# Optimization experiments

Measured on AMD Instinct MI355X. Metric: run time of the kernel, lower is better.

The kernel has to match this reference:

```python
import jax, jax.numpy as jnp
import numpy as np

B, P, ENC, DEC, EMB, ATT, FFN, V, MAXLEN = 64, 196, 512, 512, 256, 128, 1024, 2000, 160
T = MAXLEN - 1
EPS = 1e-5

def _k(i):
    return jax.random.fold_in(jax.random.key(0), i)

def _w(i, shape):
    return jax.random.normal(_k(i), shape, jnp.float32) * 0.02

def setup_inputs() -> dict:
    lens = jnp.concatenate([jnp.array([MAXLEN]), jax.random.randint(_k(2), (B - 1,), 2, MAXLEN + 1)])
    return {
        "encoder_out": jax.random.normal(_k(0), (B, P, ENC), jnp.float32),
        "encoded_captions": jax.random.randint(_k(1), (B, MAXLEN), 0, V),
        "caption_lengths": lens,
        "enc_att_w": _w(3, (ATT, ENC)), "enc_att_b": _w(4, (ATT,)),
        "dec_att_w": _w(5, (ATT, DEC)), "dec_att_b": _w(6, (ATT,)),
        "full_att_w": _w(7, (1, ATT)), "full_att_b": _w(8, (1,)),
        "gate_w1": _w(9, (ATT, DEC)), "gate_b1": _w(10, (ATT,)),
        "gate_w2": _w(11, (1, ATT)), "gate_b2": _w(12, (1,)),
        "emb": jax.random.uniform(_k(13), (V, EMB), jnp.float32, -0.1, 0.1),
        "gru1_wih": _w(14, (3 * DEC, EMB + ENC)), "gru1_whh": _w(15, (3 * DEC, DEC)),
        "gru1_bih": _w(16, (3 * DEC,)), "gru1_bhh": _w(17, (3 * DEC,)),
        "gru2_wih": _w(18, (3 * DEC, DEC)), "gru2_whh": _w(19, (3 * DEC, DEC)),
        "gru2_bih": _w(20, (3 * DEC,)), "gru2_bhh": _w(21, (3 * DEC,)),
        "proj_w": _w(22, (DEC, EMB + ENC)), "proj_b": _w(23, (DEC,)),
        "ln1_g": jnp.ones((DEC,), jnp.float32), "ln1_b": jnp.zeros((DEC,), jnp.float32),
        "ln2_g": jnp.ones((DEC,), jnp.float32), "ln2_b": jnp.zeros((DEC,), jnp.float32),
        "ffn_w1": _w(24, (FFN, DEC)), "ffn_b1": jnp.zeros((FFN,), jnp.float32),
        "ffn_w2": _w(25, (V, FFN)), "ffn_b2": jnp.zeros((V,), jnp.float32),
    }

def _gru(x, h, wih, whh, bih, bhh):
    gi = x @ wih.T + bih
    gh = h @ whh.T + bhh
    ir, iz, ig = jnp.split(gi, 3, axis=-1)
    hr, hz, hg = jnp.split(gh, 3, axis=-1)
    r = jax.nn.sigmoid(ir + hr)
    z = jax.nn.sigmoid(iz + hz)
    n = jnp.tanh(ig + r * hg)
    return (1.0 - z) * n + z * h

def _ln(x, g, b):
    m = x.mean(-1, keepdims=True)
    v = x.var(-1, keepdims=True)
    return (x - m) / jnp.sqrt(v + EPS) * g + b

def _decode(encoder_out, encoded_captions, caption_lengths,
            enc_att_w, enc_att_b, dec_att_w, dec_att_b, full_att_w, full_att_b,
            gate_w1, gate_b1, gate_w2, gate_b2, emb,
            gru1_wih, gru1_whh, gru1_bih, gru1_bhh,
            gru2_wih, gru2_whh, gru2_bih, gru2_bhh,
            proj_w, proj_b, ln1_g, ln1_b, ln2_g, ln2_b,
            ffn_w1, ffn_b1, ffn_w2, ffn_b2):
    # sort by caption length descending (packed-sequence style)
    order = jnp.argsort(-caption_lengths)
    enc = encoder_out[order]                       # [B,P,ENC]
    caps = encoded_captions[order]                 # [B,MAXLEN]
    dec_lens = caption_lengths[order] - 1          # [B]
    att1 = enc @ enc_att_w.T + enc_att_b           # [B,P,ATT] (loop-invariant)
    xs = jnp.swapaxes(emb[caps[:, :T]], 0, 1)      # [T,B,EMB] teacher forcing (p=1.0)
    masks = (jnp.arange(T)[:, None] < dec_lens[None, :]).astype(enc.dtype)  # [T,B]

    def step(carry, inp):
        h1, h2 = carry
        x_t, m = inp                               # [B,EMB], [B]
        att2 = h2 @ dec_att_w.T + dec_att_b        # [B,ATT]
        e = (jax.nn.relu(att1 + att2[:, None, :]) @ full_att_w.T + full_att_b)[..., 0]  # [B,P]
        alpha = jax.nn.softmax(e, axis=1)
        awe = jnp.einsum('bpe,bp->be', enc, alpha)
        gate = jax.nn.sigmoid(jax.nn.relu(h2 @ gate_w1.T + gate_b1) @ gate_w2.T + gate_b2)  # [B,1]
        awe = awe * gate
        gin = jnp.concatenate([x_t, awe], axis=1)  # [B,EMB+ENC]
        h1_new = _gru(gin, h1, gru1_wih, gru1_whh, gru1_bih, gru1_bhh)
        h1_res = _ln(h1_new + gin @ proj_w.T + proj_b, ln1_g, ln1_b)
        h2_new = _gru(h1_res, h2, gru2_wih, gru2_whh, gru2_bih, gru2_bhh)
        h2_res = _ln(h2_new + h1_res, ln2_g, ln2_b)  # dropout is identity (eval)
        preds = jax.nn.relu(h2_res @ ffn_w1.T + ffn_b1) @ ffn_w2.T + ffn_b2  # [B,V]
        mc = m[:, None]
        h1 = jnp.where(mc > 0, h1_new, h1)
        h2 = jnp.where(mc > 0, h2_new, h2)
        return (h1, h2), (preds * mc, alpha * mc)

    h0 = jnp.zeros((enc.shape[0], DEC), enc.dtype)
    _, (preds, alphas) = jax.lax.scan(step, (h0, h0), (xs, masks))
    predictions = jnp.swapaxes(preds, 0, 1)        # [B,T,V]
    alphas = jnp.swapaxes(alphas, 0, 1)            # [B,T,P]
    return predictions, caps, dec_lens, alphas, order

def reference(encoder_out, encoded_captions, caption_lengths,
              enc_att_w, enc_att_b, dec_att_w, dec_att_b, full_att_w, full_att_b,
              gate_w1, gate_b1, gate_w2, gate_b2, emb,
              gru1_wih, gru1_whh, gru1_bih, gru1_bhh,
              gru2_wih, gru2_whh, gru2_bih, gru2_bhh,
              proj_w, proj_b, ln1_g, ln1_b, ln2_g, ln2_b,
              ffn_w1, ffn_b1, ffn_w2, ffn_b2):
    return _decode(encoder_out, encoded_captions, caption_lengths,
                   enc_att_w, enc_att_b, dec_att_w, dec_att_b, full_att_w, full_att_b,
                   gate_w1, gate_b1, gate_w2, gate_b2, emb,
                   gru1_wih, gru1_whh, gru1_bih, gru1_bhh,
                   gru2_wih, gru2_whh, gru2_bih, gru2_bhh,
                   proj_w, proj_b, ln1_g, ln1_b, ln2_g, ln2_b,
                   ffn_w1, ffn_b1, ffn_w2, ffn_b2)
```

## Files before the change

### kernel.cpp

```cpp
#include <hip/hip_runtime.h>
#include <math.h>

#define B 64
#define P 196
#define ENCD 512
#define DECD 512
#define EMBD 256
#define ATTD 128
#define FFND 1024
#define VV 2000
#define MAXLEN 160
#define TSTEPS 159
#define EPS 1e-5f

#define OUT_PRED ((size_t)0)
#define OUT_CAPS ((size_t)(B * TSTEPS * VV))
#define OUT_DECL (OUT_CAPS + (size_t)(B * MAXLEN))
#define OUT_ALPH (OUT_DECL + (size_t)B)
#define OUT_ORDR (OUT_ALPH + (size_t)(B * TSTEPS * P))


struct Ctx {
  const float* enc; const int* caps_in; const int* lens_in;
  const float* eaw; const float* eab; const float* daw; const float* dab;
  const float* faw; const float* fab;
  const float* gw1; const float* gb1; const float* gw2; const float* gb2;
  const float* emb;
  const float* wih1; const float* whh1; const float* bih1; const float* bhh1;
  const float* wih2; const float* whh2; const float* bih2; const float* bhh2;
  const float* projw; const float* projb;
  const float* ln1g; const float* ln1b; const float* ln2g; const float* ln2b;
  const float* fw1; const float* fb1; const float* fw2; const float* fb2;
  int* leafs; int* root;
  int* order_i; int* declen; int* caps_s;
  float* EaT; float* att1;
  float* h1; float* h2; float* v1; float* v2;
  float* gin; float* fgr; float* gh1g; float* gh2g; float* att2acc;
  float* stats1; float* stats2;
  unsigned int* WA; unsigned int* WB; unsigned int* WC; unsigned int* WD;
  float* Watt;
  float* Sf; float* cbf; float* Sg; float* cbg;
  float* out;
};

__device__ __forceinline__ float sigf(float x) { return 1.f / (1.f + __expf(-x)); }

__device__ __forceinline__ float ld4(const float* p) {
  unsigned int u = __hip_atomic_load((const unsigned int*)p, __ATOMIC_RELAXED, __HIP_MEMORY_SCOPE_AGENT);
  return __uint_as_float(u);
}
__device__ __forceinline__ void st4(float* p, float v) {
  __hip_atomic_store((unsigned int*)p, __float_as_uint(v), __ATOMIC_RELAXED, __HIP_MEMORY_SCOPE_AGENT);
}
__device__ __forceinline__ void st8(float* p, float a, float b2) {
  unsigned long long v = ((unsigned long long)__float_as_uint(b2) << 32) | (unsigned long long)__float_as_uint(a);
  __hip_atomic_store((unsigned long long*)p, v, __ATOMIC_RELAXED, __HIP_MEMORY_SCOPE_AGENT);
}
__device__ __forceinline__ void atomF(float* p, float v) {
  __hip_atomic_fetch_add(p, v, __ATOMIC_RELAXED, __HIP_MEMORY_SCOPE_AGENT);
}
__device__ __forceinline__ float4 ldg16(const float* p) {
  float4 d;
  asm volatile("global_load_dwordx4 %0, %1, off sc0 sc1" : "=v"(d) : "v"(p));
  return d;
}
__device__ __forceinline__ void vmwait() { asm volatile("s_waitcnt vmcnt(0)" ::: "memory"); }

__device__ __forceinline__ unsigned short tobf(float x) {
  unsigned int u = __float_as_uint(x);
  u += 0x7fffu + ((u >> 16) & 1u);
  return (unsigned short)(u >> 16);
}
__device__ __forceinline__ float frombf(unsigned short s) {
  return __uint_as_float(((unsigned int)s) << 16);
}
__device__ __forceinline__ unsigned int pack2bf(float a, float b) {
  return (unsigned int)tobf(a) | ((unsigned int)tobf(b) << 16);
}
__device__ __forceinline__ void bf2(unsigned int u, float& a, float& b) {
  a = __uint_as_float(u << 16);
  b = __uint_as_float(u & 0xffff0000u);
}


__global__ void k_order(Ctx c) {
  __shared__ int lens[B];
  int tid = threadIdx.x;
  lens[tid] = c.lens_in[tid];
  __syncthreads();
  int li = lens[tid];
  int pos = 0;
  for (int j = 0; j < B; ++j) {
    int lj = lens[j];
    pos += (lj > li || (lj == li && j < tid)) ? 1 : 0;
  }
  c.order_i[pos] = tid;
  c.declen[pos] = li - 1;
  c.out[OUT_ORDR + pos] = (float)tid;
  c.out[OUT_DECL + pos] = (float)(li - 1);
}

__global__ __launch_bounds__(256) void k_caps(Ctx c) {
  int idx = blockIdx.x * 256 + threadIdx.x;
  if (idx < B * MAXLEN) {
    int b = idx / MAXLEN, t = idx - b * MAXLEN;
    int v = c.caps_in[c.order_i[b] * MAXLEN + t];
    c.caps_s[idx] = v;
    c.out[OUT_CAPS + idx] = (float)v;
  }
}

__global__ __launch_bounds__(256) void k_eat(Ctx c) {
  int idx = blockIdx.x * 256 + threadIdx.x;
  if (idx < 128 * 512) {
    int k = idx >> 7, d = idx & 127;
    c.EaT[(size_t)k * 128 + d] = c.eaw[(size_t)d * 512 + k];
  }
}

__global__ __launch_bounds__(256) void k_att1(Ctx c) {
  __shared__ float Xs[8 * 512];
  int tid = threadIdx.x;
  int r0 = blockIdx.x * 8;
  for (int idx = tid; idx < 8 * 512; idx += 256) {
    int rr = idx >> 9, k = idx & 511;
    int r = r0 + rr;
    int b = r / P, p = r - b * P;
    int ob = c.order_i[b];
    Xs[idx] = c.enc[((size_t)(ob * P + p)) * ENCD + k];
  }
  __syncthreads();
  int d = tid >> 1, kh = tid & 1;
  float acc[8];
#pragma unroll
  for (int rr = 0; rr < 8; ++rr) acc[rr] = 0.f;
  int kbase = kh * 256;
  for (int k = 0; k < 256; ++k) {
    float w = c.EaT[(size_t)(kbase + k) * 128 + d];
#pragma unroll
    for (int rr = 0; rr < 8; ++rr) acc[rr] = fmaf(w, Xs[rr * 512 + kbase + k], acc[rr]);
  }
#pragma unroll
  for (int rr = 0; rr < 8; ++rr) {
    acc[rr] += __shfl_xor(acc[rr], 1);
    if (kh == 0) c.att1[(size_t)(r0 + rr) * 128 + d] = acc[rr];
  }
}

__device__ __forceinline__ float wa_elem(const Ctx& c, int col, int k) {
  if (col < 1536) return c.whh1[(size_t)col * 512 + k];
  if (col < 3072) return c.whh2[(size_t)(col - 1536) * 512 + k];
  return c.ln2g[k] * c.fw1[(size_t)(col - 3072) * 512 + k];
}

__global__ __launch_bounds__(256) void k_wpa(Ctx c) {
  int s = blockIdx.x;
  unsigned int* dst = c.WA + (size_t)s * 32768;
  for (int idx = threadIdx.x; idx < 32768; idx += 256) {
    int kb8 = idx >> 9, r = idx & 511, cc = r >> 2, jw = r & 3;
    int col = s * 128 + cc, k0 = kb8 * 8 + jw * 2;
    dst[idx] = pack2bf(wa_elem(c, col, k0), wa_elem(c, col, k0 + 1));
  }
}

__device__ __forceinline__ float wb_elem(const Ctx& c, int u, int k) {
  int d = u >> 2, comp = u & 3;
  return (comp < 3) ? c.wih1[(size_t)(comp * 512 + d) * 768 + k]
                    : c.projw[(size_t)d * 768 + k];
}

__global__ __launch_bounds__(256) void k_wpb(Ctx c) {
  int s = blockIdx.x;
  unsigned int* dst = c.WB + (size_t)s * 24576;
  for (int idx = threadIdx.x; idx < 24576; idx += 256) {
    int kb8 = idx >> 8, r = idx & 255, cc = r >> 2, jw = r & 3;
    int u = s * 64 + cc, k0 = kb8 * 8 + jw * 2;
    dst[idx] = pack2bf(wb_elem(c, u, k0), wb_elem(c, u, k0 + 1));
  }
}

__device__ __forceinline__ float wc_elem(const Ctx& c, int u, int k) {
  int d = u / 3, comp = u - d * 3;
  return c.ln1g[k] * c.wih2[(size_t)(comp * 512 + d) * 512 + k];
}

__global__ __launch_bounds__(256) void k_wpc(Ctx c) {
  int s = blockIdx.x;
  unsigned int* dst = c.WC + (size_t)s * 12288;
  for (int idx = threadIdx.x; idx < 12288; idx += 256) {
    int kb8 = idx / 192, r = idx - kb8 * 192, cc = r >> 2, jw = r & 3;
    int u = s * 48 + cc, k0 = kb8 * 8 + jw * 2;
    dst[idx] = pack2bf(wc_elem(c, u, k0), wc_elem(c, u, k0 + 1));
  }
}

__device__ __forceinline__ float wd_elem(const Ctx& c, int vcol, int k) {
  return (vcol < 2000) ? c.fw2[(size_t)vcol * 1024 + k] : 0.f;
}

__global__ __launch_bounds__(256) void k_wpd(Ctx c) {
  int s = blockIdx.x;
  unsigned int* dst = c.WD + (size_t)s * 32768;
  for (int idx = threadIdx.x; idx < 32768; idx += 256) {
    int kb8 = idx >> 8, r = idx & 255, cc = r >> 2, jw = r & 3;
    int vcol = s * 64 + cc, k0 = kb8 * 8 + jw * 2;
    dst[idx] = pack2bf(wd_elem(c, vcol, k0), wd_elem(c, vcol, k0 + 1));
  }
}

__global__ __launch_bounds__(256) void k_watt(Ctx c) {
  int ks = blockIdx.x;
  float* dst = c.Watt + (size_t)ks * 16384;
  for (int idx = threadIdx.x; idx < 16384; idx += 256) {
    int kb = idx >> 10, r = idx & 1023, cc = r >> 2, jj = r & 3;
    int k = ks * 64 + kb * 4 + jj;
    dst[idx] = (cc < 128) ? c.daw[(size_t)cc * 512 + k] : c.gw1[(size_t)(cc - 128) * 512 + k];
  }
}

__global__ __launch_bounds__(256) void k_consts(Ctx c) {
  __shared__ float r1[256], r2[256];
  int i = blockIdx.x, tid = threadIdx.x;
  float a = 0.f, b2 = 0.f;
  if (i < 1024) {
    const float* w = c.fw1 + (size_t)i * 512;
    for (int k = tid; k < 512; k += 256) {
      a += frombf(tobf(c.ln2g[k] * w[k]));
      b2 = fmaf(c.ln2b[k], w[k], b2);
    }
  } else {
    const float* w = c.wih2 + (size_t)(i - 1024) * 512;
    for (int k = tid; k < 512; k += 256) {
      a += frombf(tobf(c.ln1g[k] * w[k]));
      b2 = fmaf(c.ln1b[k], w[k], b2);
    }
  }
  r1[tid] = a; r2[tid] = b2;
  __syncthreads();
  for (int s = 128; s > 0; s >>= 1) {
    if (tid < s) { r1[tid] += r1[tid + s]; r2[tid] += r2[tid + s]; }
    __syncthreads();
  }
  if (tid == 0) {
    if (i < 1024) { c.Sf[i] = r1[0]; c.cbf[i] = r2[0] + c.fb1[i]; }
    else { c.Sg[i - 1024] = r1[0]; c.cbg[i - 1024] = r2[0] + c.bih2[i - 1024]; }
  }
}


__device__ __forceinline__ void gridbar(int* leafs, int* root, int ph) {
  __builtin_amdgcn_s_waitcnt(0);
  __syncthreads();
  if (threadIdx.x == 0) {
    int old = __hip_atomic_fetch_add(&leafs[(blockIdx.x & 7) * 32], 1,
                                     __ATOMIC_RELAXED, __HIP_MEMORY_SCOPE_AGENT);
    if (old == ph * 32 - 1)
      __hip_atomic_fetch_add(root, 1, __ATOMIC_RELAXED, __HIP_MEMORY_SCOPE_AGENT);
    while (__hip_atomic_load(root, __ATOMIC_RELAXED, __HIP_MEMORY_SCOPE_AGENT) < ph * 8)
      __builtin_amdgcn_s_sleep(1);
  }
  __syncthreads();
}

__global__ __launch_bounds__(512) void persist(Ctx c) {
  __shared__ unsigned short att1L[196 * 130];
  __shared__ unsigned short encL[196 * 128];
  __shared__ float SH[12288];
  __shared__ float eL[256];
  __shared__ float alphaL[256];
  __shared__ float att2sL[128], fawL[128], dabL[128], gb1L[128], gw2L[128];
  __shared__ float wred[16];
  __shared__ float sstat[16];
  __shared__ int declenI[64];
  __shared__ float gb2v, fabv;

  const int g = blockIdx.x;
  const int tid = threadIdx.x;
  const int cg = g & 31;
  const int rg = g >> 5;
  const int r0 = rg * 8;
  const int bA = g >> 2, q = g & 3;
  const int kc = tid >> 6;
  const int ct = tid & 63;

  if (tid < 128) {
    fawL[tid] = c.faw[tid];
    dabL[tid] = c.dab[tid] + c.eab[tid];
    gb1L[tid] = c.gb1[tid];
    gw2L[tid] = c.gw2[tid];
  }
  if (tid == 0) { gb2v = c.gb2[0]; fabv = c.fab[0]; }
  if (tid < 64) declenI[tid] = c.declen[tid];
  {
    const int ob = c.order_i[bA];
    for (int idx = tid; idx < 196 * 128; idx += 512) {
      int p = idx >> 7, j = idx & 127;
      att1L[p * 130 + j] = tobf(c.att1[((size_t)bA * P + p) * 128 + j]);
      encL[idx] = tobf(c.enc[((size_t)(ob * P + p)) * 512 + q * 128 + j]);
    }
  }
  __syncthreads();

  int ph = 0;
  for (int t = 0; t < MAXLEN; ++t) {
    {
      float* XS = SH;
      float* RED = SH + 4096;
      const float* hsrc = ((cg < 12) ? c.h1 : (cg < 24) ? c.h2 : c.v2) + (size_t)r0 * 512;
      float4 s0 = ldg16(hsrc + tid * 4);
      float4 s1 = ldg16(hsrc + 2048 + tid * 4);
      if (tid < 8) {
        int slot = (t + 1) & 1;
        float a = ld4(c.stats2 + slot * 128 + (r0 + tid) * 2);
        float b2 = ld4(c.stats2 + slot * 128 + (r0 + tid) * 2 + 1);
        float m = a * (1.f / 512.f);
        float va = b2 * (1.f / 512.f) - m * m;
        sstat[tid] = m; sstat[8 + tid] = rsqrtf(va + EPS);
      }
      vmwait();
      *(float4*)(XS + tid * 4) = s0;
      *(float4*)(XS + 2048 + tid * 4) = s1;
      __syncthreads();

      {
        const unsigned int* wp = c.WA + (size_t)cg * 32768 + (size_t)kc * 4096 + ct * 4;
        const float* xb = XS + kc * 64;
        float acc[8][2];
#pragma unroll
        for (int r = 0; r < 8; ++r) { acc[r][0] = 0.f; acc[r][1] = 0.f; }
#pragma unroll 2
        for (int i = 0; i < 8; ++i) {
          uint4 u0 = *(const uint4*)(wp + i * 512);
          uint4 u1 = *(const uint4*)(wp + i * 512 + 256);
          float wa[8], wb[8];
          bf2(u0.x, wa[0], wa[1]); bf2(u0.y, wa[2], wa[3]);
          bf2(u0.z, wa[4], wa[5]); bf2(u0.w, wa[6], wa[7]);
          bf2(u1.x, wb[0], wb[1]); bf2(u1.y, wb[2], wb[3]);
          bf2(u1.z, wb[4], wb[5]); bf2(u1.w, wb[6], wb[7]);
#pragma unroll
          for (int r = 0; r < 8; ++r) {
            float4 x0 = *(const float4*)(xb + r * 512 + i * 8);
            float4 x1 = *(const float4*)(xb + r * 512 + i * 8 + 4);
            acc[r][0] = fmaf(wa[0], x0.x, fmaf(wa[1], x0.y, fmaf(wa[2], x0.z, fmaf(wa[3], x0.w, acc[r][0]))));
            acc[r][0] = fmaf(wa[4], x1.x, fmaf(wa[5], x1.y, fmaf(wa[6], x1.z, fmaf(wa[7], x1.w, acc[r][0]))));
            acc[r][1] = fmaf(wb[0], x0.x, fmaf(wb[1], x0.y, fmaf(wb[2], x0.z, fmaf(wb[3], x0.w, acc[r][1]))));
            acc[r][1] = fmaf(wb[4], x1.x, fmaf(wb[5], x1.y, fmaf(wb[6], x1.z, fmaf(wb[7], x1.w, acc[r][1]))));
          }
        }
#pragma unroll
        for (int r = 0; r < 8; ++r) {
          RED[(kc * 8 + r) * 128 + ct] = acc[r][0];
          RED[(kc * 8 + r) * 128 + ct + 64] = acc[r][1];
        }
      }
      if (cg >= 16 && cg < 24) {
        const int ks_att = cg - 16;
        const int ct2 = tid >> 1, half = tid & 1;
        const float* wp = c.Watt + (size_t)ks_att * 16384 + half * 8192 + ct2 * 4;
        const float* xb = XS + ks_att * 64 + half * 32;
        float a[8];
#pragma unroll
        for (int r = 0; r < 8; ++r) a[r] = 0.f;
#pragma unroll
        for (int i = 0; i < 8; ++i) {
          float4 w = *(const float4*)(wp + i * 1024);
#pragma unroll
          for (int r = 0; r < 8; ++r) {
            float4 x = *(const float4*)(xb + r * 512 + i * 4);
            a[r] = fmaf(w.x, x.x, fmaf(w.y, x.y, fmaf(w.z, x.z, fmaf(w.w, x.w, a[r]))));
          }
        }
#pragma unroll
        for (int r = 0; r < 8; ++r) {
          a[r] += __shfl_xor(a[r], 1);
          if (half == 0) atomF(c.att2acc + (r0 + r) * 256 + ct2, a[r]);
        }
      }
      __syncthreads();
      {
        int row = tid >> 6, cp = (tid & 63) * 2;
        float s0_ = 0.f, s1_ = 0.f;
#pragma unroll
        for (int k8 = 0; k8 < 8; ++k8) {
          float2 v = *(const float2*)(RED + (k8 * 8 + row) * 128 + cp);
          s0_ += v.x; s1_ += v.y;
        }
        int bb = r0 + row;
        int gcol = cg * 128 + cp;
        if (cg < 12) st8(c.gh1g + bb * 1536 + gcol, s0_, s1_);
        else if (cg < 24) st8(c.gh2g + bb * 1536 + (gcol - 1536), s0_, s1_);
        else {
          int cf = gcol - 3072;
          float m2 = sstat[row], i2 = sstat[8 + row];
          float v0 = i2 * (s0_ - m2 * c.Sf[cf]) + c.cbf[cf];
          float v1v = i2 * (s1_ - m2 * c.Sf[cf + 1]) + c.cbf[cf + 1];
          st8(c.fgr + bb * 1024 + cf, fmaxf(v0, 0.f), fmaxf(v1v, 0.f));
        }
      }
    }
    gridbar(c.leafs, c.root, ++ph);

    {
      float* XS = SH;
      float* RED = SH + 8192;
      const float* fsrc = c.fgr + (size_t)r0 * 1024;
      float4 s0 = ldg16(fsrc + tid * 4);
      float4 s1 = ldg16(fsrc + 2048 + tid * 4);
      float4 s2 = ldg16(fsrc + 4096 + tid * 4);
      float4 s3 = ldg16(fsrc + 6144 + tid * 4);
      float a2r = 0.f, g1r = 0.f;
      if (tid < 128) {
        a2r = ld4(c.att2acc + bA * 256 + tid);
        g1r = ld4(c.att2acc + bA * 256 + 128 + tid);
      }
      if (g == 0) {
        int sl = t & 1;
        if (tid < 128) st4(c.stats1 + sl * 128 + tid, 0.f);
        else if (tid < 256) st4(c.stats2 + sl * 128 + (tid - 128), 0.f);
      }
      vmwait();
      *(float4*)(XS + tid * 4) = s0;
      *(float4*)(XS + 2048 + tid * 4) = s1;
      *(float4*)(XS + 4096 + tid * 4) = s2;
      *(float4*)(XS + 6144 + tid * 4) = s3;
      if (tid < 128) {
        att2sL[tid] = a2r + dabL[tid];
        float g1 = fmaxf(g1r + gb1L[tid], 0.f);
        float gv = g1 * gw2L[tid];
#pragma unroll
        for (int w = 1; w < 64; w <<= 1) gv += __shfl_xor(gv, w);
        if ((tid & 63) == 0) wred[tid >> 6] = gv;
      }
      __syncthreads();

      {
        const unsigned int* wp = c.WD + (size_t)cg * 32768 + (size_t)kc * 4096 + ct * 4;
        const float* xb = XS + kc * 128;
        float acc[8];
#pragma unroll
        for (int r = 0; r < 8; ++r) acc[r] = 0.f;
#pragma unroll 4
        for (int i = 0; i < 16; ++i) {
          uint4 u = *(const uint4*)(wp + i * 256);
          float w8[8];
          bf2(u.x, w8[0], w8[1]); bf2(u.y, w8[2], w8[3]);
          bf2(u.z, w8[4], w8[5]); bf2(u.w, w8[6], w8[7]);
#pragma unroll
          for (int r = 0; r < 8; ++r) {
            float4 x0 = *(const float4*)(xb + r * 1024 + i * 8);
            float4 x1 = *(const float4*)(xb + r * 1024 + i * 8 + 4);
            acc[r] = fmaf(w8[0], x0.x, fmaf(w8[1], x0.y, fmaf(w8[2], x0.z, fmaf(w8[3], x0.w, acc[r]))));
            acc[r] = fmaf(w8[4], x1.x, fmaf(w8[5], x1.y, fmaf(w8[6], x1.z, fmaf(w8[7], x1.w, acc[r]))));
          }
        }
#pragma unroll
        for (int r = 0; r < 8; ++r) RED[(kc * 8 + r) * 64 + ct] = acc[r];
      }
      __syncthreads();
      {
        int row = tid >> 6, cl = tid & 63;
        float s = 0.f;
#pragma unroll
        for (int k8 = 0; k8 < 8; ++k8) s += RED[(k8 * 8 + row) * 64 + cl];
        int bb = r0 + row, vcol = cg * 64 + cl;
        if (vcol < 2000 && t > 0 && (t - 1) < declenI[bb])
          c.out[OUT_PRED + ((size_t)bb * TSTEPS + (t - 1)) * VV + vcol] = s + c.fb2[vcol];
      }
      {
        int p = tid >> 1, jh = tid & 1;
        float e = 0.f;
        if (p < 196) {
          const unsigned short* ap = att1L + p * 130 + jh * 64;
#pragma unroll 8
          for (int j = 0; j < 64; ++j)
            e = fmaf(fmaxf(frombf(ap[j]) + att2sL[jh * 64 + j], 0.f), fawL[jh * 64 + j], e);
        }
        e += __shfl_xor(e, 1);
        if (jh == 0 && p < 196) eL[p] = e + fabv;
      }
      __syncthreads();
      float ev = (tid < 196) ? eL[tid] : -3.0e38f;
      if (tid < 256) {
        float mv = ev;
#pragma unroll
        for (int w = 1; w < 64; w <<= 1) mv = fmaxf(mv, __shfl_xor(mv, w));
        if ((tid & 63) == 0) wred[2 + (tid >> 6)] = mv;
      }
      __syncthreads();
      float mx = fmaxf(fmaxf(wred[2], wred[3]), fmaxf(wred[4], wred[5]));
      float ex = (tid < 196) ? __expf(ev - mx) : 0.f;
      if (tid < 256) {
        float sv = ex;
#pragma unroll
        for (int w = 1; w < 64; w <<= 1) sv += __shfl_xor(sv, w);
        if ((tid & 63) == 0) wred[6 + (tid >> 6)] = sv;
      }
      __syncthreads();
      float inv = 1.f / (wred[6] + wred[7] + wred[8] + wred[9]);
      float gate = sigf(wred[0] + wred[1] + gb2v);
      if (tid < 256) alphaL[tid] = ex * inv;
      if (q == 0 && tid < 196 && t < declenI[bA])
        c.out[OUT_ALPH + ((size_t)bA * TSTEPS + t) * P + tid] = ex * inv;
      __syncthreads();
      {
        int el = tid & 127, pq = tid >> 7;
        const unsigned short* ep2 = encL + (size_t)(pq * 49) * 128 + el;
        const float* alp = alphaL + pq * 49;
        float s_ = 0.f;
#pragma unroll
        for (int i = 0; i < 49; ++i) s_ = fmaf(alp[i], frombf(ep2[(size_t)i * 128]), s_);
        RED[tid] = s_;
      }
      __syncthreads();
      if (tid < 128) {
        float aw = RED[tid] + RED[128 + tid] + RED[256 + tid] + RED[384 + tid];
        st4(c.gin + bA * 768 + 256 + q * 128 + tid, aw * gate);
      }
      if (q == 1 && tid < 256) {
        int tok = c.caps_s[bA * MAXLEN + t];
        st4(c.gin + bA * 768 + tid, c.emb[(size_t)tok * 256 + tid]);
      }
    }
    gridbar(c.leafs, c.root, ++ph);

    {
      float* XS = SH;
      float* RED = SH + 6144;
      const float* gsrc = c.gin + (size_t)r0 * 768;
      float4 s0 = ldg16(gsrc + tid * 4);
      float4 s1 = ldg16(gsrc + 2048 + tid * 4);
      float4 s2 = ldg16(gsrc + 4096 + tid * 4);
      if (g < 32) st4(c.att2acc + g * 512 + tid, 0.f);
      vmwait();
      *(float4*)(XS + tid * 4) = s0;
      *(float4*)(XS + 2048 + tid * 4) = s1;
      *(float4*)(XS + 4096 + tid * 4) = s2;
      __syncthreads();

      {
        const unsigned int* wp = c.WB + (size_t)cg * 24576 + (size_t)kc * 3072 + ct * 4;
        const float* xb = XS + kc * 96;
        float acc[8];
#pragma unroll
        for (int r = 0; r < 8; ++r) acc[r] = 0.f;
#pragma unroll 4
        for (int i = 0; i < 12; ++i) {
          uint4 u = *(const uint4*)(wp + i * 256);
          float w8[8];
          bf2(u.x, w8[0], w8[1]); bf2(u.y, w8[2], w8[3]);
          bf2(u.z, w8[4], w8[5]); bf2(u.w, w8[6], w8[7]);
#pragma unroll
          for (int r = 0; r < 8; ++r) {
            float4 x0 = *(const float4*)(xb + r * 768 + i * 8);
            float4 x1 = *(const float4*)(xb + r * 768 + i * 8 + 4);
            acc[r] = fmaf(w8[0], x0.x, fmaf(w8[1], x0.y, fmaf(w8[2], x0.z, fmaf(w8[3], x0.w, acc[r]))));
            acc[r] = fmaf(w8[4], x1.x, fmaf(w8[5], x1.y, fmaf(w8[6], x1.z, fmaf(w8[7], x1.w, acc[r]))));
          }
        }
#pragma unroll
        for (int r = 0; r < 8; ++r) RED[(kc * 8 + r) * 64 + ct] = acc[r];
      }
      __syncthreads();
      if (tid < 128) {
        int row = tid >> 4, dl = tid & 15;
        int bb = r0 + row, d = cg * 16 + dl;
        float gi0 = 0.f, gi1 = 0.f, gi2v = 0.f, gi3 = 0.f;
#pragma unroll
        for (int k8 = 0; k8 < 8; ++k8) {
          float4 v = *(const float4*)(RED + (k8 * 8 + row) * 64 + dl * 4);
          gi0 += v.x; gi1 += v.y; gi2v += v.z; gi3 += v.w;
        }
        float gir = gi0 + c.bih1[d];
        float giz = gi1 + c.bih1[512 + d];
        float gig = gi2v + c.bih1[1024 + d];
        float pj = gi3 + c.projb[d];
        float hr = ld4(c.gh1g + bb * 1536 + d) + c.bhh1[d];
        float hz = ld4(c.gh1g + bb * 1536 + 512 + d) + c.bhh1[512 + d];
        float hg = ld4(c.gh1g + bb * 1536 + 1024 + d) + c.bhh1[1024 + d];
        float r_ = sigf(gir + hr);
        float z_ = sigf(giz + hz);
        float n_ = tanhf(gig + r_ * hg);
        float hold = ld4(c.h1 + bb * 512 + d);
        float hnew = (1.f - z_) * n_ + z_ * hold;
        st4(c.h1 + bb * 512 + d, (t < declenI[bb]) ? hnew : hold);
        float v1v = hnew + pj;
        st4(c.v1 + bb * 512 + d, v1v);
        float ss = v1v, sq = v1v * v1v;
#pragma unroll
        for (int w = 1; w < 16; w <<= 1) { ss += __shfl_xor(ss, w); sq += __shfl_xor(sq, w); }
        if (dl == 0) {
          atomF(c.stats1 + (t & 1) * 128 + bb * 2, ss);
          atomF(c.stats1 + (t & 1) * 128 + bb * 2 + 1, sq);
        }
      }
    }
    gridbar(c.leafs, c.root, ++ph);

    {
      float* XS = SH;
      float* RED = SH + 4096;
      const float* vsrc = c.v1 + (size_t)r0 * 512;
      float4 s0 = ldg16(vsrc + tid * 4);
      float4 s1 = ldg16(vsrc + 2048 + tid * 4);
      if (tid < 8) {
        float a = ld4(c.stats1 + (t & 1) * 128 + (r0 + tid) * 2);
        float b2 = ld4(c.stats1 + (t & 1) * 128 + (r0 + tid) * 2 + 1);
        float m = a * (1.f / 512.f);
        float va = b2 * (1.f / 512.f) - m * m;
        sstat[tid] = m; sstat[8 + tid] = rsqrtf(va + EPS);
      }
      vmwait();
      *(float4*)(XS + tid * 4) = s0;
      *(float4*)(XS + 2048 + tid * 4) = s1;
      __syncthreads();

      if (ct < 48) {
        const unsigned int* wp = c.WC + (size_t)cg * 12288 + (size_t)kc * 1536 + ct * 4;
        const float* xb = XS + kc * 64;
        float acc[8];
#pragma unroll
        for (int r = 0; r < 8; ++r) acc[r] = 0.f;
#pragma unroll 2
        for (int i = 0; i < 8; ++i) {
          uint4 u = *(const uint4*)(wp + i * 192);
          float w8[8];
          bf2(u.x, w8[0], w8[1]); bf2(u.y, w8[2], w8[3]);
          bf2(u.z, w8[4], w8[5]); bf2(u.w, w8[6], w8[7]);
#pragma unroll
          for (int r = 0; r < 8; ++r) {
            float4 x0 = *(const float4*)(xb + r * 512 + i * 8);
            float4 x1 = *(const float4*)(xb + r * 512 + i * 8 + 4);
            acc[r] = fmaf(w8[0], x0.x, fmaf(w8[1], x0.y, fmaf(w8[2], x0.z, fmaf(w8[3], x0.w, acc[r]))));
            acc[r] = fmaf(w8[4], x1.x, fmaf(w8[5], x1.y, fmaf(w8[6], x1.z, fmaf(w8[7], x1.w, acc[r]))));
          }
        }
#pragma unroll
        for (int r = 0; r < 8; ++r) RED[(kc * 8 + r) * 48 + ct] = acc[r];
      }
      __syncthreads();
      if (tid < 128) {
        int row = tid >> 4, dl = tid & 15;
        int bb = r0 + row, d = cg * 16 + dl;
        float gi0 = 0.f, gi1 = 0.f, gi2v = 0.f;
#pragma unroll
        for (int k8 = 0; k8 < 8; ++k8) {
          const float* rp = RED + (k8 * 8 + row) * 48 + dl * 3;
          gi0 += rp[0]; gi1 += rp[1]; gi2v += rp[2];
        }
        float m1 = sstat[row], i1 = sstat[8 + row];
        float gir = i1 * (gi0 - m1 * c.Sg[d]) + c.cbg[d];
        float giz = i1 * (gi1 - m1 * c.Sg[512 + d]) + c.cbg[512 + d];
        float gig = i1 * (gi2v - m1 * c.Sg[1024 + d]) + c.cbg[1024 + d];
        float hr = ld4(c.gh2g + bb * 1536 + d) + c.bhh2[d];
        float hz = ld4(c.gh2g + bb * 1536 + 512 + d) + c.bhh2[512 + d];
        float hg = ld4(c.gh2g + bb * 1536 + 1024 + d) + c.bhh2[1024 + d];
        float r_ = sigf(gir + hr);
        float z_ = sigf(giz + hz);
        float n_ = tanhf(gig + r_ * hg);
        float hold = ld4(c.h2 + bb * 512 + d);
        float hnew = (1.f - z_) * n_ + z_ * hold;
        st4(c.h2 + bb * 512 + d, (t < declenI[bb]) ? hnew : hold);
        float h1r = (XS[row * 512 + d] - m1) * i1 * c.ln1g[d] + c.ln1b[d];
        float v2v = hnew + h1r;
        st4(c.v2 + bb * 512 + d, v2v);
        float ss = v2v, sq = v2v * v2v;
#pragma unroll
        for (int w = 1; w < 16; w <<= 1) { ss += __shfl_xor(ss, w); sq += __shfl_xor(sq, w); }
        if (dl == 0) {
          atomF(c.stats2 + (t & 1) * 128 + bb * 2, ss);
          atomF(c.stats2 + (t & 1) * 128 + bb * 2 + 1, sq);
        }
      }
    }
    gridbar(c.leafs, c.root, ++ph);
  }
}

extern "C" void kernel_launch(void* const* d_in, const int* in_sizes, int n_in,
                              void* d_out, int out_size, void* d_ws, size_t ws_size,
                              hipStream_t stream) {
  (void)in_sizes; (void)n_in; (void)ws_size;
  Ctx c;
  c.enc = (const float*)d_in[0];
  c.caps_in = (const int*)d_in[1];
  c.lens_in = (const int*)d_in[2];
  c.eaw = (const float*)d_in[3];
  c.eab = (const float*)d_in[4];
  c.daw = (const float*)d_in[5];
  c.dab = (const float*)d_in[6];
  c.faw = (const float*)d_in[7];
  c.fab = (const float*)d_in[8];
  c.gw1 = (const float*)d_in[9];
  c.gb1 = (const float*)d_in[10];
  c.gw2 = (const float*)d_in[11];
  c.gb2 = (const float*)d_in[12];
  c.emb = (const float*)d_in[13];
  c.wih1 = (const float*)d_in[14];
  c.whh1 = (const float*)d_in[15];
  c.bih1 = (const float*)d_in[16];
  c.bhh1 = (const float*)d_in[17];
  c.wih2 = (const float*)d_in[18];
  c.whh2 = (const float*)d_in[19];
  c.bih2 = (const float*)d_in[20];
  c.bhh2 = (const float*)d_in[21];
  c.projw = (const float*)d_in[22];
  c.projb = (const float*)d_in[23];
  c.ln1g = (const float*)d_in[24];
  c.ln1b = (const float*)d_in[25];
  c.ln2g = (const float*)d_in[26];
  c.ln2b = (const float*)d_in[27];
  c.fw1 = (const float*)d_in[28];
  c.fb1 = (const float*)d_in[29];
  c.fw2 = (const float*)d_in[30];
  c.fb2 = (const float*)d_in[31];
  c.out = (float*)d_out;

  char* wp_ = (char*)d_ws;
  auto alloc = [&](size_t bytes) -> char* {
    char* p = wp_;
    wp_ += (bytes + 255) & ~(size_t)255;
    return p;
  };
  char* zbase = wp_;
  c.leafs = (int*)alloc(256 * 4);
  c.root = (int*)alloc(256);
  c.h1 = (float*)alloc((size_t)B * 512 * 4);
  c.h2 = (float*)alloc((size_t)B * 512 * 4);
  c.stats1 = (float*)alloc(2 * 64 * 2 * 4);
  c.stats2 = (float*)alloc(2 * 64 * 2 * 4);
  c.att2acc = (float*)alloc((size_t)B * 256 * 4);
  c.v2 = (float*)alloc((size_t)B * 512 * 4);
  size_t zbytes = (size_t)(wp_ - zbase);

  c.order_i = (int*)alloc(B * 4);
  c.declen = (int*)alloc(B * 4);
  c.caps_s = (int*)alloc((size_t)B * MAXLEN * 4);
  c.EaT = (float*)alloc((size_t)512 * 128 * 4);
  c.att1 = (float*)alloc((size_t)B * P * 128 * 4);
  c.v1 = (float*)alloc((size_t)B * 512 * 4);
  c.gin = (float*)alloc((size_t)B * 768 * 4);
  c.fgr = (float*)alloc((size_t)B * 1024 * 4);
  c.gh1g = (float*)alloc((size_t)B * 1536 * 4);
  c.gh2g = (float*)alloc((size_t)B * 1536 * 4);
  c.WA = (unsigned int*)alloc((size_t)32 * 32768 * 4);
  c.WB = (unsigned int*)alloc((size_t)32 * 24576 * 4);
  c.WC = (unsigned int*)alloc((size_t)32 * 12288 * 4);
  c.WD = (unsigned int*)alloc((size_t)32 * 32768 * 4);
  c.Watt = (float*)alloc((size_t)8 * 16384 * 4);
  c.Sf = (float*)alloc(1024 * 4);
  c.cbf = (float*)alloc(1024 * 4);
  c.Sg = (float*)alloc(1536 * 4);
  c.cbg = (float*)alloc(1536 * 4);

  hipMemsetAsync(d_out, 0, (size_t)out_size * 4, stream);
  hipMemsetAsync(zbase, 0, zbytes, stream);

  k_order<<<1, 64, 0, stream>>>(c);
  k_caps<<<(B * MAXLEN + 255) / 256, 256, 0, stream>>>(c);
  k_eat<<<(128 * 512 + 255) / 256, 256, 0, stream>>>(c);
  k_att1<<<(B * P) / 8, 256, 0, stream>>>(c);
  k_wpa<<<32, 256, 0, stream>>>(c);
  k_wpb<<<32, 256, 0, stream>>>(c);
  k_wpc<<<32, 256, 0, stream>>>(c);
  k_wpd<<<32, 256, 0, stream>>>(c);
  k_watt<<<8, 256, 0, stream>>>(c);
  k_consts<<<2560, 256, 0, stream>>>(c);

  persist<<<256, 512, 0, stream>>>(c);
}
```

Before: 11.72 ms.

## Double persistent kernel block size, splitting batch rows across thread halves

Grows the persistent kernel from 512 to 1024 threads per block. Each thread now computes 4 of the 8 batch rows in the bf16 matvec phases, so per-thread accumulator count and serial work are halved. Reduction and epilogue steps are restricted to the first 512 threads. Every thread still loads the same weights, so global weight traffic per block doubles, and the 1024-thread launch bound squeezes the register budget, which risks spills and lower wave occupancy.

```diff
diff --git a/kernel.cpp b/kernel.cpp
--- a/kernel.cpp
+++ b/kernel.cpp
@@ -262,7 +262,7 @@
   __syncthreads();
 }
 
-__global__ __launch_bounds__(512) void persist(Ctx c) {
+__global__ __launch_bounds__(1024) void persist(Ctx c) {
   __shared__ unsigned short att1L[196 * 130];
   __shared__ unsigned short encL[196 * 128];
   __shared__ float SH[12288];
@@ -280,7 +280,8 @@
   const int rg = g >> 5;
   const int r0 = rg * 8;
   const int bA = g >> 2, q = g & 3;
-  const int kc = tid >> 6;
+  const int kc = (tid >> 6) & 7;
+  const int rh = tid >> 9;
   const int ct = tid & 63;
 
   if (tid < 128) {
@@ -293,7 +294,7 @@
   if (tid < 64) declenI[tid] = c.declen[tid];
   {
     const int ob = c.order_i[bA];
-    for (int idx = tid; idx < 196 * 128; idx += 512) {
+    for (int idx = tid; idx < 196 * 128; idx += 1024) {
       int p = idx >> 7, j = idx & 127;
       att1L[p * 130 + j] = tobf(c.att1[((size_t)bA * P + p) * 128 + j]);
       encL[idx] = tobf(c.enc[((size_t)(ob * P + p)) * 512 + q * 128 + j]);
@@ -307,8 +308,7 @@
       float* XS = SH;
       float* RED = SH + 4096;
       const float* hsrc = ((cg < 12) ? c.h1 : (cg < 24) ? c.h2 : c.v2) + (size_t)r0 * 512;
-      float4 s0 = ldg16(hsrc + tid * 4);
-      float4 s1 = ldg16(hsrc + 2048 + tid * 4);
+      float4 sA = ldg16(hsrc + tid * 4);
       if (tid < 8) {
         int slot = (t + 1) & 1;
         float a = ld4(c.stats2 + slot * 128 + (r0 + tid) * 2);
@@ -318,16 +318,15 @@
         sstat[tid] = m; sstat[8 + tid] = rsqrtf(va + EPS);
       }
       vmwait();
-      *(float4*)(XS + tid * 4) = s0;
-      *(float4*)(XS + 2048 + tid * 4) = s1;
+      *(float4*)(XS + tid * 4) = sA;
       __syncthreads();
 
       {
         const unsigned int* wp = c.WA + (size_t)cg * 32768 + (size_t)kc * 4096 + ct * 4;
-        const float* xb = XS + kc * 64;
-        float acc[8][2];
-#pragma unroll
-        for (int r = 0; r < 8; ++r) { acc[r][0] = 0.f; acc[r][1] = 0.f; }
+        const float* xb = XS + (rh * 4) * 512 + kc * 64;
+        float acc[4][2];
+#pragma unroll
+        for (int r = 0; r < 4; ++r) { acc[r][0] = 0.f; acc[r][1] = 0.f; }
 #pragma unroll 2
         for (int i = 0; i < 8; ++i) {
           uint4 u0 = *(const uint4*)(wp + i * 512);
@@ -338,7 +337,7 @@
           bf2(u1.x, wb[0], wb[1]); bf2(u1.y, wb[2], wb[3]);
           bf2(u1.z, wb[4], wb[5]); bf2(u1.w, wb[6], wb[7]);
 #pragma unroll
-          for (int r = 0; r < 8; ++r) {
+          for (int r = 0; r < 4; ++r) {
             float4 x0 = *(const float4*)(xb + r * 512 + i * 8);
             float4 x1 = *(const float4*)(xb + r * 512 + i * 8 + 4);
             acc[r][0] = fmaf(wa[0], x0.x, fmaf(wa[1], x0.y, fmaf(wa[2], x0.z, fmaf(wa[3], x0.w, acc[r][0]))));
@@ -348,12 +347,12 @@
           }
         }
 #pragma unroll
-        for (int r = 0; r < 8; ++r) {
-          RED[(kc * 8 + r) * 128 + ct] = acc[r][0];
-          RED[(kc * 8 + r) * 128 + ct + 64] = acc[r][1];
-        }
-      }
-      if (cg >= 16 && cg < 24) {
+        for (int r = 0; r < 4; ++r) {
+          RED[(kc * 8 + rh * 4 + r) * 128 + ct] = acc[r][0];
+          RED[(kc * 8 + rh * 4 + r) * 128 + ct + 64] = acc[r][1];
+        }
+      }
+      if (cg >= 16 && cg < 24 && tid < 512) {
         const int ks_att = cg - 16;
         const int ct2 = tid >> 1, half = tid & 1;
         const float* wp = c.Watt + (size_t)ks_att * 16384 + half * 8192 + ct2 * 4;
@@ -377,7 +376,7 @@
         }
       }
       __syncthreads();
-      {
+      if (tid < 512) {
         int row = tid >> 6, cp = (tid & 63) * 2;
         float s0_ = 0.f, s1_ = 0.f;
 #pragma unroll
@@ -405,9 +404,7 @@
       float* RED = SH + 8192;
       const float* fsrc = c.fgr + (size_t)r0 * 1024;
       float4 s0 = ldg16(fsrc + tid * 4);
-      float4 s1 = ldg16(fsrc + 2048 + tid * 4);
-      float4 s2 = ldg16(fsrc + 4096 + tid * 4);
-      float4 s3 = ldg16(fsrc + 6144 + tid * 4);
+      float4 s1 = ldg16(fsrc + 4096 + tid * 4);
       float a2r = 0.f, g1r = 0.f;
       if (tid < 128) {
         a2r = ld4(c.att2acc + bA * 256 + tid);
@@ -420,9 +417,7 @@
       }
       vmwait();
       *(float4*)(XS + tid * 4) = s0;
-      *(float4*)(XS + 2048 + tid * 4) = s1;
-      *(float4*)(XS + 4096 + tid * 4) = s2;
-      *(float4*)(XS + 6144 + tid * 4) = s3;
+      *(float4*)(XS + 4096 + tid * 4) = s1;
       if (tid < 128) {
         att2sL[tid] = a2r + dabL[tid];
         float g1 = fmaxf(g1r + gb1L[tid], 0.f);
@@ -435,10 +430,10 @@
 
       {
         const unsigned int* wp = c.WD + (size_t)cg * 32768 + (size_t)kc * 4096 + ct * 4;
-        const float* xb = XS + kc * 128;
-        float acc[8];
-#pragma unroll
-        for (int r = 0; r < 8; ++r) acc[r] = 0.f;
+        const float* xb = XS + (rh * 4) * 1024 + kc * 128;
+        float acc[4];
+#pragma unroll
+        for (int r = 0; r < 4; ++r) acc[r] = 0.f;
 #pragma unroll 4
         for (int i = 0; i < 16; ++i) {
           uint4 u = *(const uint4*)(wp + i * 256);
@@ -446,7 +441,7 @@
           bf2(u.x, w8[0], w8[1]); bf2(u.y, w8[2], w8[3]);
           bf2(u.z, w8[4], w8[5]); bf2(u.w, w8[6], w8[7]);
 #pragma unroll
-          for (int r = 0; r < 8; ++r) {
+          for (int r = 0; r < 4; ++r) {
             float4 x0 = *(const float4*)(xb + r * 1024 + i * 8);
             float4 x1 = *(const float4*)(xb + r * 1024 + i * 8 + 4);
             acc[r] = fmaf(w8[0], x0.x, fmaf(w8[1], x0.y, fmaf(w8[2], x0.z, fmaf(w8[3], x0.w, acc[r]))));
@@ -454,10 +449,10 @@
           }
         }
 #pragma unroll
-        for (int r = 0; r < 8; ++r) RED[(kc * 8 + r) * 64 + ct] = acc[r];
-      }
-      __syncthreads();
-      {
+        for (int r = 0; r < 4; ++r) RED[(kc * 8 + rh * 4 + r) * 64 + ct] = acc[r];
+      }
+      __syncthreads();
+      if (tid < 512) {
         int row = tid >> 6, cl = tid & 63;
         float s = 0.f;
 #pragma unroll
@@ -502,7 +497,7 @@
       if (q == 0 && tid < 196 && t < declenI[bA])
         c.out[OUT_ALPH + ((size_t)bA * TSTEPS + t) * P + tid] = ex * inv;
       __syncthreads();
-      {
+      if (tid < 512) {
         int el = tid & 127, pq = tid >> 7;
         const unsigned short* ep2 = encL + (size_t)(pq * 49) * 128 + el;
         const float* alp = alphaL + pq * 49;
@@ -528,21 +523,20 @@
       float* RED = SH + 6144;
       const float* gsrc = c.gin + (size_t)r0 * 768;
       float4 s0 = ldg16(gsrc + tid * 4);
-      float4 s1 = ldg16(gsrc + 2048 + tid * 4);
-      float4 s2 = ldg16(gsrc + 4096 + tid * 4);
-      if (g < 32) st4(c.att2acc + g * 512 + tid, 0.f);
+      float4 s1;
+      if (tid < 512) s1 = ldg16(gsrc + 4096 + tid * 4);
+      if (g < 32 && tid < 512) st4(c.att2acc + g * 512 + tid, 0.f);
       vmwait();
       *(float4*)(XS + tid * 4) = s0;
-      *(float4*)(XS + 2048 + tid * 4) = s1;
-      *(float4*)(XS + 4096 + tid * 4) = s2;
+      if (tid < 512) *(float4*)(XS + 4096 + tid * 4) = s1;
       __syncthreads();
 
       {
         const unsigned int* wp = c.WB + (size_t)cg * 24576 + (size_t)kc * 3072 + ct * 4;
-        const float* xb = XS + kc * 96;
-        float acc[8];
-#pragma unroll
-        for (int r = 0; r < 8; ++r) acc[r] = 0.f;
+        const float* xb = XS + (rh * 4) * 768 + kc * 96;
+        float acc[4];
+#pragma unroll
+        for (int r = 0; r < 4; ++r) acc[r] = 0.f;
 #pragma unroll 4
         for (int i = 0; i < 12; ++i) {
           uint4 u = *(const uint4*)(wp + i * 256);
@@ -550,7 +544,7 @@
           bf2(u.x, w8[0], w8[1]); bf2(u.y, w8[2], w8[3]);
           bf2(u.z, w8[4], w8[5]); bf2(u.w, w8[6], w8[7]);
 #pragma unroll
-          for (int r = 0; r < 8; ++r) {
+          for (int r = 0; r < 4; ++r) {
             float4 x0 = *(const float4*)(xb + r * 768 + i * 8);
             float4 x1 = *(const float4*)(xb + r * 768 + i * 8 + 4);
             acc[r] = fmaf(w8[0], x0.x, fmaf(w8[1], x0.y, fmaf(w8[2], x0.z, fmaf(w8[3], x0.w, acc[r]))));
@@ -558,7 +552,7 @@
           }
         }
 #pragma unroll
-        for (int r = 0; r < 8; ++r) RED[(kc * 8 + r) * 64 + ct] = acc[r];
+        for (int r = 0; r < 4; ++r) RED[(kc * 8 + rh * 4 + r) * 64 + ct] = acc[r];
       }
       __syncthreads();
       if (tid < 128) {
@@ -600,8 +594,7 @@
       float* XS = SH;
       float* RED = SH + 4096;
       const float* vsrc = c.v1 + (size_t)r0 * 512;
-      float4 s0 = ldg16(vsrc + tid * 4);
-      float4 s1 = ldg16(vsrc + 2048 + tid * 4);
+      float4 sA = ldg16(vsrc + tid * 4);
       if (tid < 8) {
         float a = ld4(c.stats1 + (t & 1) * 128 + (r0 + tid) * 2);
         float b2 = ld4(c.stats1 + (t & 1) * 128 + (r0 + tid) * 2 + 1);
@@ -610,16 +603,15 @@
         sstat[tid] = m; sstat[8 + tid] = rsqrtf(va + EPS);
       }
       vmwait();
-      *(float4*)(XS + tid * 4) = s0;
-      *(float4*)(XS + 2048 + tid * 4) = s1;
+      *(float4*)(XS + tid * 4) = sA;
       __syncthreads();
 
       if (ct < 48) {
         const unsigned int* wp = c.WC + (size_t)cg * 12288 + (size_t)kc * 1536 + ct * 4;
-        const float* xb = XS + kc * 64;
-        float acc[8];
-#pragma unroll
-        for (int r = 0; r < 8; ++r) acc[r] = 0.f;
+        const float* xb = XS + (rh * 4) * 512 + kc * 64;
+        float acc[4];
+#pragma unroll
+        for (int r = 0; r < 4; ++r) acc[r] = 0.f;
 #pragma unroll 2
         for (int i = 0; i < 8; ++i) {
           uint4 u = *(const uint4*)(wp + i * 192);
@@ -627,7 +619,7 @@
           bf2(u.x, w8[0], w8[1]); bf2(u.y, w8[2], w8[3]);
           bf2(u.z, w8[4], w8[5]); bf2(u.w, w8[6], w8[7]);
 #pragma unroll
-          for (int r = 0; r < 8; ++r) {
+          for (int r = 0; r < 4; ++r) {
             float4 x0 = *(const float4*)(xb + r * 512 + i * 8);
             float4 x1 = *(const float4*)(xb + r * 512 + i * 8 + 4);
             acc[r] = fmaf(w8[0], x0.x, fmaf(w8[1], x0.y, fmaf(w8[2], x0.z, fmaf(w8[3], x0.w, acc[r]))));
@@ -635,7 +627,7 @@
           }
         }
 #pragma unroll
-        for (int r = 0; r < 8; ++r) RED[(kc * 8 + r) * 48 + ct] = acc[r];
+        for (int r = 0; r < 4; ++r) RED[(kc * 8 + rh * 4 + r) * 48 + ct] = acc[r];
       }
       __syncthreads();
       if (tid < 128) {
@@ -766,5 +758,5 @@
   k_watt<<<8, 256, 0, stream>>>(c);
   k_consts<<<2560, 256, 0, stream>>>(c);
 
-  persist<<<256, 512, 0, stream>>>(c);
-}
+  persist<<<256, 1024, 0, stream>>>(c);
+}
```

Result: slower. 13.83 ms (+18.0%).
